# Kernel tuning notes

Hardware: AMD Instinct MI355X
Metric: run time of the kernel (lower is better)

The kernel has to match this reference:

```python
import jax, jax.numpy as jnp
import numpy as np

# Per-level grid spatial shapes: ceil([T,H,W]/grid_size/2**i) + 1 with
# video (T,H,W) = (120,1080,1920), grid_size=8, n_levels=2.
GRID_SHAPES = [jnp.array([16.0, 136.0, 241.0], dtype=jnp.float32),
               jnp.array([9.0, 69.0, 121.0], dtype=jnp.float32)]
EMB_DIM = 16
N_PTS = 1_000_000

# 8 binary corner offsets, MSB-first bit order (matches f'{i:03b}').
OFFSETS = jnp.array([[(i >> 2) & 1, (i >> 1) & 1, i & 1] for i in range(8)],
                    dtype=jnp.float32)  # [8,3]


def setup_inputs() -> dict:
    key = jax.random.key(0)
    k0, k1, k2 = jax.random.split(key, 3)
    inputs = jax.random.uniform(k0, (N_PTS, 3), dtype=jnp.float32)
    emb0 = jax.random.normal(k1, (16, 136, 241, EMB_DIM), dtype=jnp.float32)
    emb1 = jax.random.normal(k2, (9, 69, 121, EMB_DIM), dtype=jnp.float32)
    return {"inputs": inputs, "emb0": emb0, "emb1": emb1}


def _encode_level(inputs, emb, gshape):
    # inputs: [N,3] in [0,1]; emb: [T,H,W,D]; gshape: [3] float grid shape
    coords = inputs * (gshape - 1.0)                         # [N,3]
    corner = jnp.floor(coords[:, None, :] + OFFSETS)         # [N,8,3]
    corner = jnp.clip(corner, 0.0, gshape - 1.0)             # [N,8,3]
    idx = corner.astype(jnp.int32)
    values = emb[idx[..., 0], idx[..., 1], idx[..., 2]]      # [N,8,D] gather
    weights = jnp.prod(1.0 - jnp.abs(corner - coords[:, None, :]),
                       axis=-1, keepdims=True)               # [N,8,1]
    return jnp.sum(weights * values, axis=-2)                # [N,D]


def reference(inputs, emb0, emb1):
    out0 = _encode_level(inputs, emb0, GRID_SHAPES[0])
    out1 = _encode_level(inputs, emb1, GRID_SHAPES[1])
    return jnp.concatenate([out0, out1], axis=-1)            # [N, 2*D]
```

## Files before the change

### kernel.cpp

```cpp
#include <hip/hip_runtime.h>


typedef float floatx4 __attribute__((ext_vector_type(4)));

#define KXB 8
#define KYB 17
#define KZB 31
#define NBINS (KXB * KYB * KZB)
#define NSUB 4
#define CAPS 104
#define CAP_TOT (NSUB * CAPS)
#define CNT_DWORDS (NSUB * NBINS + 1)

#define L0X 3
#define L0Y 9
#define L0Z 9
#define L0CELLS (L0X * L0Y * L0Z)
#define CSTR 20

__device__ __forceinline__ int point_key(float px, float py, float pz) {
    int ix = (int)(px * 15.0f);  ix = min(max(ix, 0), 15);
    int iy = (int)(py * 135.0f); iy = min(max(iy, 0), 135);
    int iz = (int)(pz * 240.0f); iz = min(max(iz, 0), 240);
    return ((ix >> 1) * KYB + (iy >> 3)) * KZB + (iz >> 3);
}

__device__ __forceinline__ void load4pts(const float* __restrict__ pts, int i4,
                                         float px[4], float py[4], float pz[4]) {
    const floatx4* v = (const floatx4*)(pts + (size_t)i4 * 3);
    const floatx4 a = v[0], b = v[1], c = v[2];
    px[0] = a.x; py[0] = a.y; pz[0] = a.z;
    px[1] = a.w; py[1] = b.x; pz[1] = b.y;
    px[2] = b.z; py[2] = b.w; pz[2] = c.x;
    px[3] = c.y; py[3] = c.z; pz[3] = c.w;
}

__global__ __launch_bounds__(256)
void k_zero(unsigned* __restrict__ cnt) {
    const int i = blockIdx.x * blockDim.x + threadIdx.x;
    if (i < CNT_DWORDS) cnt[i] = 0u;
}

__global__ __launch_bounds__(256)
void k_bin(const float* __restrict__ pts, int n,
           unsigned* __restrict__ cnt, unsigned* __restrict__ ovfc,
           unsigned* __restrict__ slots, unsigned* __restrict__ ovf) {
    const int i4 = (blockIdx.x * blockDim.x + threadIdx.x) * 4;
    if (i4 >= n) return;
    if (i4 + 3 < n) {
        float px[4], py[4], pz[4];
        load4pts(pts, i4, px, py, pz);
        int k[4];
#pragma unroll
        for (int j = 0; j < 4; ++j) k[j] = point_key(px[j], py[j], pz[j]);
        unsigned pos[4];
#pragma unroll
        for (int j = 0; j < 4; ++j)
            pos[j] = atomicAdd(&cnt[j * NBINS + k[j]], 1u);
#pragma unroll
        for (int j = 0; j < 4; ++j) {
            if (pos[j] < CAPS)
                slots[(size_t)k[j] * CAP_TOT + j * CAPS + pos[j]] = (unsigned)(i4 + j);
            else
                ovf[atomicAdd(ovfc, 1u)] = (unsigned)(i4 + j);
        }
    } else {
        for (int j = 0; j < 4 && i4 + j < n; ++j) {
            const size_t b = (size_t)(i4 + j) * 3;
            const int k = point_key(pts[b], pts[b+1], pts[b+2]);
            const unsigned pos = atomicAdd(&cnt[j * NBINS + k], 1u);
            if (pos < CAPS) slots[(size_t)k * CAP_TOT + j * CAPS + pos] = (unsigned)(i4 + j);
            else            ovf[atomicAdd(ovfc, 1u)] = (unsigned)(i4 + j);
        }
    }
}

__device__ __forceinline__ void setup_lds(float cx, float cy, float cz,
                                          int xb, int yb, int zb, int d,
                                          int* __restrict__ off,
                                          float* __restrict__ w) {
    float gx[2] = { floorf(cx), floorf(cx + 1.0f) };
    float gy[2] = { floorf(cy), floorf(cy + 1.0f) };
    float gz[2] = { floorf(cz), floorf(cz + 1.0f) };
    float wx[2], wy[2], wz[2];
    int   xo[2], yo[2], zo[2];
#pragma unroll
    for (int b = 0; b < 2; ++b) {
        gx[b] = fminf(fmaxf(gx[b], 0.0f), 15.0f);
        gy[b] = fminf(fmaxf(gy[b], 0.0f), 135.0f);
        gz[b] = fminf(fmaxf(gz[b], 0.0f), 240.0f);
        wx[b] = 1.0f - fabsf(gx[b] - cx);
        wy[b] = 1.0f - fabsf(gy[b] - cy);
        wz[b] = 1.0f - fabsf(gz[b] - cz);
        xo[b] = min((int)gx[b] - xb, L0X - 1) * (L0Y * L0Z * CSTR);
        yo[b] = min((int)gy[b] - yb, L0Y - 1) * (L0Z * CSTR);
        zo[b] = min((int)gz[b] - zb, L0Z - 1) * CSTR + d;
    }
    float wyz[4];
    int   yzo[4];
#pragma unroll
    for (int j = 0; j < 2; ++j)
#pragma unroll
        for (int k = 0; k < 2; ++k) {
            wyz[2 * j + k] = wy[j] * wz[k];
            yzo[2 * j + k] = yo[j] + zo[k];
        }
#pragma unroll
    for (int c = 0; c < 8; ++c) {
        const int i = (c >> 2) & 1, jk = c & 3;
        w[c]   = wx[i] * wyz[jk];
        off[c] = xo[i] + yzo[jk];
    }
}

__device__ __forceinline__ void setup_glb(float cx, float cy, float cz,
                                          float tm1, float hm1, float wm1,
                                          int sh, int sw, int d,
                                          int* __restrict__ off,
                                          float* __restrict__ w) {
    float gx[2] = { floorf(cx), floorf(cx + 1.0f) };
    float gy[2] = { floorf(cy), floorf(cy + 1.0f) };
    float gz[2] = { floorf(cz), floorf(cz + 1.0f) };
    float wx[2], wy[2], wz[2];
    int   xo[2], yo[2], zo[2];
#pragma unroll
    for (int b = 0; b < 2; ++b) {
        gx[b] = fminf(fmaxf(gx[b], 0.0f), tm1);
        gy[b] = fminf(fmaxf(gy[b], 0.0f), hm1);
        gz[b] = fminf(fmaxf(gz[b], 0.0f), wm1);
        wx[b] = 1.0f - fabsf(gx[b] - cx);
        wy[b] = 1.0f - fabsf(gy[b] - cy);
        wz[b] = 1.0f - fabsf(gz[b] - cz);
        xo[b] = (int)gx[b] * sh;
        yo[b] = (int)gy[b] * sw;
        zo[b] = (int)gz[b] * 16 + d;
    }
    float wyz[4];
    int   yzo[4];
#pragma unroll
    for (int j = 0; j < 2; ++j)
#pragma unroll
        for (int k = 0; k < 2; ++k) {
            wyz[2 * j + k] = wy[j] * wz[k];
            yzo[2 * j + k] = yo[j] + zo[k];
        }
#pragma unroll
    for (int c = 0; c < 8; ++c) {
        const int i = (c >> 2) & 1, jk = c & 3;
        w[c]   = wx[i] * wyz[jk];
        off[c] = xo[i] + yzo[jk];
    }
}

__device__ __forceinline__ void encode_glb_quad(int p, int lane4,
                                                const float* __restrict__ pts,
                                                const float* __restrict__ emb0,
                                                const float* __restrict__ emb1,
                                                float* __restrict__ out) {
    const size_t b = (size_t)p * 3;
    const float px = pts[b], py = pts[b + 1], pz = pts[b + 2];
    int   o0[8], o1[8];
    float w0[8], w1[8];
    setup_glb(px * 15.0f, py * 135.0f, pz * 240.0f, 15.0f, 135.0f, 240.0f,
              136 * 241 * 16, 241 * 16, lane4, o0, w0);
    setup_glb(px * 8.0f, py * 68.0f, pz * 120.0f, 8.0f, 68.0f, 120.0f,
              69 * 121 * 16, 121 * 16, lane4, o1, w1);
    floatx4 a0 = {0,0,0,0}, a1 = {0,0,0,0};
#pragma unroll
    for (int c = 0; c < 8; ++c) a0 += w0[c] * *(const floatx4*)(emb0 + o0[c]);
#pragma unroll
    for (int c = 0; c < 8; ++c) a1 += w1[c] * *(const floatx4*)(emb1 + o1[c]);
    float* row = out + (size_t)p * 32 + lane4;
    __builtin_nontemporal_store(a0, (floatx4*)row);
    __builtin_nontemporal_store(a1, (floatx4*)(row + 16));
}

__global__ __launch_bounds__(256, 4)
void k_main_bins(const unsigned* __restrict__ slots,
                 const unsigned* __restrict__ cnt,
                 const unsigned* __restrict__ ovfc,
                 const unsigned* __restrict__ ovf,
                 const float* __restrict__ pts,
                 const float* __restrict__ emb0,
                 const float* __restrict__ emb1,
                 float* __restrict__ out) {
    const int bin = (blockIdx.x & 7) * 527 + (blockIdx.x >> 3);
    const unsigned n0 = min(cnt[bin],             (unsigned)CAPS);
    const unsigned n1 = min(cnt[NBINS + bin],     (unsigned)CAPS);
    const unsigned n2 = min(cnt[2 * NBINS + bin], (unsigned)CAPS);
    const unsigned n3 = min(cnt[3 * NBINS + bin], (unsigned)CAPS);
    const unsigned c0 = n0, c1 = c0 + n1, c2 = c1 + n2, nt = c2 + n3;

    __shared__ float lds0[L0CELLS * CSTR];

    const int tid = threadIdx.x;
    const int d = (tid & 3) * 4;

    if (nt != 0) {
        const int bz = bin % KZB;
        const int t1 = bin / KZB;
        const int by = t1 % KYB;
        const int bx = t1 / KYB;

        const int x0 = bx * 2, y0 = by * 8, z0 = bz * 8;

        for (int idx = tid; idx < L0CELLS * 4; idx += 256) {
            const int cell = idx >> 2, q = (idx & 3) * 4;
            const int lz = cell % L0Z;
            const int t = cell / L0Z;
            const int ly = t % L0Y, lx = t / L0Y;
            const int gx = min(x0 + lx, 15), gy = min(y0 + ly, 135), gz = min(z0 + lz, 240);
            const floatx4 v = *(const floatx4*)(emb0 + ((size_t)(gx * 136 + gy) * 241 + gz) * 16 + q);
            *(floatx4*)(lds0 + cell * CSTR + q) = v;
        }
        __syncthreads();

        const int quad = tid >> 2;
        const size_t sbase = (size_t)bin * CAP_TOT;

        auto slot_of = [&](unsigned t) -> unsigned {
            const unsigned seg = (t >= c0) + (t >= c1) + (t >= c2);
            const unsigned base = (seg == 0) ? 0u : ((seg == 1) ? c0 : ((seg == 2) ? c1 : c2));
            return (unsigned)(sbase + seg * CAPS + (t - base));
        };

        unsigned tA = quad, tB = quad + 64;
        int origA = (int)slots[slot_of(min(tA, nt - 1))];
        int origB = (int)slots[slot_of(min(tB, nt - 1))];
        size_t pbA = (size_t)origA * 3;
        float pxA = pts[pbA], pyA = pts[pbA + 1], pzA = pts[pbA + 2];

        while (tA < nt) {
            const unsigned tC = tB + 64;
            const int origC = (int)slots[slot_of(min(tC, nt - 1))];
            const size_t pbB = (size_t)origB * 3;
            const float pxB = pts[pbB], pyB = pts[pbB + 1], pzB = pts[pbB + 2];

            int   o0[8], o1[8];
            float w0[8], w1[8];
            setup_lds(pxA * 15.0f, pyA * 135.0f, pzA * 240.0f, x0, y0, z0, d, o0, w0);
            setup_glb(pxA * 8.0f, pyA * 68.0f, pzA * 120.0f, 8.0f, 68.0f, 120.0f,
                      69 * 121 * 16, 121 * 16, d, o1, w1);

            floatx4 v1[8];
#pragma unroll
            for (int c = 0; c < 8; ++c) v1[c] = *(const floatx4*)(emb1 + o1[c]);
            __builtin_amdgcn_sched_barrier(0);

            floatx4 a0 = {0.f, 0.f, 0.f, 0.f}, a1 = {0.f, 0.f, 0.f, 0.f};
#pragma unroll
            for (int c = 0; c < 8; ++c) a0 += w0[c] * *(const floatx4*)(lds0 + o0[c]);
#pragma unroll
            for (int c = 0; c < 8; ++c) a1 += w1[c] * v1[c];

            float* row = out + (size_t)origA * 32 + d;
            __builtin_nontemporal_store(a0, (floatx4*)row);
            __builtin_nontemporal_store(a1, (floatx4*)(row + 16));

            tA = tB; tB = tC;
            origA = origB; origB = origC;
            pxA = pxB; pyA = pyB; pzA = pzB;
        }
    }

    if (blockIdx.x < 64) {
        const unsigned total = *ovfc;
        for (unsigned i = (blockIdx.x * 256 + tid) >> 2; i < total;
             i += (64u * 256u) >> 2) {
            encode_glb_quad((int)ovf[i], d, pts, emb0, emb1, out);
        }
    }
}

__global__ __launch_bounds__(256)
void k_main_plain(const float* __restrict__ pts,
                  const float* __restrict__ emb0,
                  const float* __restrict__ emb1,
                  float* __restrict__ out, int n) {
    const int g = blockIdx.x * blockDim.x + threadIdx.x;
    const int p = g >> 2;
    if (p >= n) return;
    encode_glb_quad(p, (g & 3) * 4, pts, emb0, emb1, out);
}

extern "C" void kernel_launch(void* const* d_in, const int* in_sizes, int n_in,
                              void* d_out, int out_size, void* d_ws, size_t ws_size,
                              hipStream_t stream) {
    const float* pts  = (const float*)d_in[0];
    const float* emb0 = (const float*)d_in[1];
    const float* emb1 = (const float*)d_in[2];
    float* out = (float*)d_out;
    const int n = in_sizes[0] / 3;

    const int block = 256;
    const int n4      = (n + 3) / 4;
    const int grid_p4 = (n4 + block - 1) / block;
    const int grid_4l = (int)(((long long)n * 4 + block - 1) / block);
    const int grid_z  = (CNT_DWORDS + block - 1) / block;

    const size_t off_cnt   = 0;
    const size_t off_ovfc  = (size_t)NSUB * NBINS * 4;
    const size_t off_slots = ((off_ovfc + 4 + 31) & ~(size_t)31);
    const size_t off_ovf   = off_slots + (size_t)NBINS * CAP_TOT * 4;
    const size_t need      = off_ovf + (size_t)n * 4;

    if (ws_size < need) {
        k_main_plain<<<grid_4l, block, 0, stream>>>(pts, emb0, emb1, out, n);
        return;
    }

    char* ws = (char*)d_ws;
    unsigned* cnt   = (unsigned*)(ws + off_cnt);
    unsigned* ovfc  = (unsigned*)(ws + off_ovfc);
    unsigned* slots = (unsigned*)(ws + off_slots);
    unsigned* ovf   = (unsigned*)(ws + off_ovf);

    k_zero<<<grid_z, block, 0, stream>>>(cnt);
    k_bin<<<grid_p4, block, 0, stream>>>(pts, n, cnt, ovfc, slots, ovf);
    k_main_bins<<<NBINS, block, 0, stream>>>(slots, cnt, ovfc, ovf,
                                             pts, emb0, emb1, out);
}
```

Baseline: 111.3 us.

## Process pairs of x-adjacent bins per block with shared LDS tile and deeper prefetch

Each block now handles two bins adjacent in x, staging a larger level-0 embedding tile (5 x-planes instead of 3) in LDS once for both, which halves the block count and cuts redundant tile loads. The inner loop is restructured into a ping-pong of two point states, so the global emb1 gathers for the next point are issued before the current point is consumed. The cost is more registers per thread (two full states with 8 floatx4 each), which may reduce occupancy, plus a larger LDS footprint and fewer blocks for load balancing.

```diff
diff --git a/kernel.cpp b/kernel.cpp
--- a/kernel.cpp
+++ b/kernel.cpp
@@ -7,12 +7,13 @@
 #define KYB 17
 #define KZB 31
 #define NBINS (KXB * KYB * KZB)
+#define NPAIRS (NBINS / 2)
 #define NSUB 4
 #define CAPS 104
 #define CAP_TOT (NSUB * CAPS)
 #define CNT_DWORDS (NSUB * NBINS + 1)
 
-#define L0X 3
+#define L0X 5
 #define L0Y 9
 #define L0Z 9
 #define L0CELLS (L0X * L0Y * L0Z)
@@ -175,6 +176,43 @@
     __builtin_nontemporal_store(a1, (floatx4*)(row + 16));
 }
 
+struct PtS {
+    float   px, py, pz;
+    int     orig;
+    float   w1[8];
+    floatx4 v1[8];
+};
+
+__device__ __forceinline__ void pt_load(PtS& s, unsigned slotaddr,
+                                        const unsigned* __restrict__ slots,
+                                        const float* __restrict__ pts,
+                                        const float* __restrict__ emb1, int d) {
+    s.orig = (int)slots[slotaddr];
+    const size_t pb = (size_t)s.orig * 3;
+    s.px = pts[pb]; s.py = pts[pb + 1]; s.pz = pts[pb + 2];
+    int o1[8];
+    setup_glb(s.px * 8.0f, s.py * 68.0f, s.pz * 120.0f, 8.0f, 68.0f, 120.0f,
+              69 * 121 * 16, 121 * 16, d, o1, s.w1);
+#pragma unroll
+    for (int c = 0; c < 8; ++c) s.v1[c] = *(const floatx4*)(emb1 + o1[c]);
+}
+
+__device__ __forceinline__ void pt_consume(const PtS& s, int x0, int y0, int z0,
+                                           int d, const float* __restrict__ lds0,
+                                           float* __restrict__ out) {
+    int   o0[8];
+    float w0[8];
+    setup_lds(s.px * 15.0f, s.py * 135.0f, s.pz * 240.0f, x0, y0, z0, d, o0, w0);
+    floatx4 a0 = {0.f, 0.f, 0.f, 0.f}, a1 = {0.f, 0.f, 0.f, 0.f};
+#pragma unroll
+    for (int c = 0; c < 8; ++c) a0 += w0[c] * *(const floatx4*)(lds0 + o0[c]);
+#pragma unroll
+    for (int c = 0; c < 8; ++c) a1 += s.w1[c] * s.v1[c];
+    float* row = out + (size_t)s.orig * 32 + d;
+    __builtin_nontemporal_store(a0, (floatx4*)row);
+    __builtin_nontemporal_store(a1, (floatx4*)(row + 16));
+}
+
 __global__ __launch_bounds__(256, 4)
 void k_main_bins(const unsigned* __restrict__ slots,
                  const unsigned* __restrict__ cnt,
@@ -184,82 +222,64 @@
                  const float* __restrict__ emb0,
                  const float* __restrict__ emb1,
                  float* __restrict__ out) {
-    const int bin = (blockIdx.x & 7) * 527 + (blockIdx.x >> 3);
-    const unsigned n0 = min(cnt[bin],             (unsigned)CAPS);
-    const unsigned n1 = min(cnt[NBINS + bin],     (unsigned)CAPS);
-    const unsigned n2 = min(cnt[2 * NBINS + bin], (unsigned)CAPS);
-    const unsigned n3 = min(cnt[3 * NBINS + bin], (unsigned)CAPS);
-    const unsigned c0 = n0, c1 = c0 + n1, c2 = c1 + n2, nt = c2 + n3;
+    const int xcd = blockIdx.x & 7, ib = blockIdx.x >> 3;
+    const int pair = (xcd < 4) ? (xcd * 264 + ib) : (4 * 264 + (xcd - 4) * 263 + ib);
+
+    const int bxp  = pair / (KYB * KZB);
+    const int rest = pair % (KYB * KZB);
+    const int by = rest / KZB, bz = rest % KZB;
+    const int binA = (2 * bxp) * (KYB * KZB) + rest;
+
+    const int x0 = bxp * 4, y0 = by * 8, z0 = bz * 8;
 
     __shared__ float lds0[L0CELLS * CSTR];
 
     const int tid = threadIdx.x;
     const int d = (tid & 3) * 4;
 
-    if (nt != 0) {
-        const int bz = bin % KZB;
-        const int t1 = bin / KZB;
-        const int by = t1 % KYB;
-        const int bx = t1 / KYB;
-
-        const int x0 = bx * 2, y0 = by * 8, z0 = bz * 8;
-
-        for (int idx = tid; idx < L0CELLS * 4; idx += 256) {
-            const int cell = idx >> 2, q = (idx & 3) * 4;
-            const int lz = cell % L0Z;
-            const int t = cell / L0Z;
-            const int ly = t % L0Y, lx = t / L0Y;
-            const int gx = min(x0 + lx, 15), gy = min(y0 + ly, 135), gz = min(z0 + lz, 240);
-            const floatx4 v = *(const floatx4*)(emb0 + ((size_t)(gx * 136 + gy) * 241 + gz) * 16 + q);
-            *(floatx4*)(lds0 + cell * CSTR + q) = v;
-        }
-        __syncthreads();
-
-        const int quad = tid >> 2;
+    for (int idx = tid; idx < L0CELLS * 4; idx += 256) {
+        const int cell = idx >> 2, q = (idx & 3) * 4;
+        const int lz = cell % L0Z;
+        const int t = cell / L0Z;
+        const int ly = t % L0Y, lx = t / L0Y;
+        const int gx = min(x0 + lx, 15), gy = min(y0 + ly, 135), gz = min(z0 + lz, 240);
+        const floatx4 v = *(const floatx4*)(emb0 + ((size_t)(gx * 136 + gy) * 241 + gz) * 16 + q);
+        *(floatx4*)(lds0 + cell * CSTR + q) = v;
+    }
+    __syncthreads();
+
+    const int quad = tid >> 2;
+
+#pragma unroll 1
+    for (int sub = 0; sub < 2; ++sub) {
+        const int bin = binA + sub * (KYB * KZB);
+        const unsigned n0 = min(cnt[bin],             (unsigned)CAPS);
+        const unsigned n1 = min(cnt[NBINS + bin],     (unsigned)CAPS);
+        const unsigned n2 = min(cnt[2 * NBINS + bin], (unsigned)CAPS);
+        const unsigned n3 = min(cnt[3 * NBINS + bin], (unsigned)CAPS);
+        const unsigned c0 = n0, c1 = c0 + n1, c2 = c1 + n2, nt = c2 + n3;
+        if (nt == 0) continue;
+
         const size_t sbase = (size_t)bin * CAP_TOT;
-
         auto slot_of = [&](unsigned t) -> unsigned {
             const unsigned seg = (t >= c0) + (t >= c1) + (t >= c2);
             const unsigned base = (seg == 0) ? 0u : ((seg == 1) ? c0 : ((seg == 2) ? c1 : c2));
             return (unsigned)(sbase + seg * CAPS + (t - base));
         };
 
-        unsigned tA = quad, tB = quad + 64;
-        int origA = (int)slots[slot_of(min(tA, nt - 1))];
-        int origB = (int)slots[slot_of(min(tB, nt - 1))];
-        size_t pbA = (size_t)origA * 3;
-        float pxA = pts[pbA], pyA = pts[pbA + 1], pzA = pts[pbA + 2];
-
-        while (tA < nt) {
-            const unsigned tC = tB + 64;
-            const int origC = (int)slots[slot_of(min(tC, nt - 1))];
-            const size_t pbB = (size_t)origB * 3;
-            const float pxB = pts[pbB], pyB = pts[pbB + 1], pzB = pts[pbB + 2];
-
-            int   o0[8], o1[8];
-            float w0[8], w1[8];
-            setup_lds(pxA * 15.0f, pyA * 135.0f, pzA * 240.0f, x0, y0, z0, d, o0, w0);
-            setup_glb(pxA * 8.0f, pyA * 68.0f, pzA * 120.0f, 8.0f, 68.0f, 120.0f,
-                      69 * 121 * 16, 121 * 16, d, o1, w1);
-
-            floatx4 v1[8];
-#pragma unroll
-            for (int c = 0; c < 8; ++c) v1[c] = *(const floatx4*)(emb1 + o1[c]);
+        PtS sA, sB;
+        unsigned t = quad;
+        pt_load(sA, slot_of(min(t, nt - 1)), slots, pts, emb1, d);
+        while (t < nt) {
+            pt_load(sB, slot_of(min(t + 64, nt - 1)), slots, pts, emb1, d);
             __builtin_amdgcn_sched_barrier(0);
-
-            floatx4 a0 = {0.f, 0.f, 0.f, 0.f}, a1 = {0.f, 0.f, 0.f, 0.f};
-#pragma unroll
-            for (int c = 0; c < 8; ++c) a0 += w0[c] * *(const floatx4*)(lds0 + o0[c]);
-#pragma unroll
-            for (int c = 0; c < 8; ++c) a1 += w1[c] * v1[c];
-
-            float* row = out + (size_t)origA * 32 + d;
-            __builtin_nontemporal_store(a0, (floatx4*)row);
-            __builtin_nontemporal_store(a1, (floatx4*)(row + 16));
-
-            tA = tB; tB = tC;
-            origA = origB; origB = origC;
-            pxA = pxB; pyA = pyB; pzA = pzB;
+            pt_consume(sA, x0, y0, z0, d, lds0, out);
+            t += 64;
+            if (t >= nt) break;
+            pt_load(sA, slot_of(min(t + 64, nt - 1)), slots, pts, emb1, d);
+            __builtin_amdgcn_sched_barrier(0);
+            pt_consume(sB, x0, y0, z0, d, lds0, out);
+            t += 64;
         }
     }
 
@@ -317,6 +337,6 @@
 
     k_zero<<<grid_z, block, 0, stream>>>(cnt);
     k_bin<<<grid_p4, block, 0, stream>>>(pts, n, cnt, ovfc, slots, ovf);
-    k_main_bins<<<NBINS, block, 0, stream>>>(slots, cnt, ovfc, ovf,
-                                             pts, emb0, emb1, out);
-}
+    k_main_bins<<<NPAIRS, block, 0, stream>>>(slots, cnt, ovfc, ovf,
+                                              pts, emb0, emb1, out);
+}
```

After: 130.4 us. 1.17x slower.

## Software-pipeline level-1 gathers one iteration ahead with double-buffered registers

Applied to the files above, without the earlier changes.

Restructures the per-bin point loop into a deeper software pipeline. The level-1 emb1 gather for the next point is issued before the current point's LDS interpolation and store, using two alternating register buffers, with slot and coordinate prefetch extended to three points ahead. The aim is to hide global gather latency behind the LDS work. In exchange it uses more VGPRs, which can lower occupancy, and it computes setup_glb twice per point.

```diff
diff --git a/kernel.cpp b/kernel.cpp
--- a/kernel.cpp
+++ b/kernel.cpp
@@ -201,7 +201,6 @@
         const int t1 = bin / KZB;
         const int by = t1 % KYB;
         const int bx = t1 / KYB;
-
         const int x0 = bx * 2, y0 = by * 8, z0 = bz * 8;
 
         for (int idx = tid; idx < L0CELLS * 4; idx += 256) {
@@ -224,42 +223,68 @@
             return (unsigned)(sbase + seg * CAPS + (t - base));
         };
 
-        unsigned tA = quad, tB = quad + 64;
-        int origA = (int)slots[slot_of(min(tA, nt - 1))];
-        int origB = (int)slots[slot_of(min(tB, nt - 1))];
-        size_t pbA = (size_t)origA * 3;
-        float pxA = pts[pbA], pyA = pts[pbA + 1], pzA = pts[pbA + 2];
-
-        while (tA < nt) {
-            const unsigned tC = tB + 64;
-            const int origC = (int)slots[slot_of(min(tC, nt - 1))];
-            const size_t pbB = (size_t)origB * 3;
-            const float pxB = pts[pbB], pyB = pts[pbB + 1], pzB = pts[pbB + 2];
-
-            int   o0[8], o1[8];
+        auto consume = [&](int orig, float px_, float py_, float pz_,
+                           const floatx4* v1) {
+            int   o0[8], o1u[8];
             float w0[8], w1[8];
-            setup_lds(pxA * 15.0f, pyA * 135.0f, pzA * 240.0f, x0, y0, z0, d, o0, w0);
-            setup_glb(pxA * 8.0f, pyA * 68.0f, pzA * 120.0f, 8.0f, 68.0f, 120.0f,
-                      69 * 121 * 16, 121 * 16, d, o1, w1);
-
-            floatx4 v1[8];
-#pragma unroll
-            for (int c = 0; c < 8; ++c) v1[c] = *(const floatx4*)(emb1 + o1[c]);
-            __builtin_amdgcn_sched_barrier(0);
-
+            setup_lds(px_ * 15.0f, py_ * 135.0f, pz_ * 240.0f, x0, y0, z0, d, o0, w0);
+            setup_glb(px_ * 8.0f, py_ * 68.0f, pz_ * 120.0f, 8.0f, 68.0f, 120.0f,
+                      69 * 121 * 16, 121 * 16, d, o1u, w1);
             floatx4 a0 = {0.f, 0.f, 0.f, 0.f}, a1 = {0.f, 0.f, 0.f, 0.f};
 #pragma unroll
             for (int c = 0; c < 8; ++c) a0 += w0[c] * *(const floatx4*)(lds0 + o0[c]);
 #pragma unroll
             for (int c = 0; c < 8; ++c) a1 += w1[c] * v1[c];
-
-            float* row = out + (size_t)origA * 32 + d;
+            float* row = out + (size_t)orig * 32 + d;
             __builtin_nontemporal_store(a0, (floatx4*)row);
             __builtin_nontemporal_store(a1, (floatx4*)(row + 16));
-
-            tA = tB; tB = tC;
-            origA = origB; origB = origC;
-            pxA = pxB; pyA = pyB; pzA = pzB;
+        };
+
+        auto issue_v1 = [&](float px_, float py_, float pz_, floatx4* v1) {
+            int o1[8]; float wt[8];
+            setup_glb(px_ * 8.0f, py_ * 68.0f, pz_ * 120.0f, 8.0f, 68.0f, 120.0f,
+                      69 * 121 * 16, 121 * 16, d, o1, wt);
+#pragma unroll
+            for (int c = 0; c < 8; ++c) v1[c] = *(const floatx4*)(emb1 + o1[c]);
+        };
+
+        unsigned t = quad;
+        int origA = (int)slots[slot_of(min(t,       nt - 1))];
+        int origB = (int)slots[slot_of(min(t + 64,  nt - 1))];
+        int origC = (int)slots[slot_of(min(t + 128, nt - 1))];
+        size_t pb = (size_t)origA * 3;
+        float pxA = pts[pb], pyA = pts[pb + 1], pzA = pts[pb + 2];
+        pb = (size_t)origB * 3;
+        float pxB = pts[pb], pyB = pts[pb + 1], pzB = pts[pb + 2];
+        floatx4 v1A[8], v1B[8];
+        if (t < nt) issue_v1(pxA, pyA, pzA, v1A);
+
+        while (t < nt) {
+            {
+                const int origD = (int)slots[slot_of(min(t + 192, nt - 1))];
+                pb = (size_t)origC * 3;
+                const float pxC = pts[pb], pyC = pts[pb + 1], pzC = pts[pb + 2];
+                issue_v1(pxB, pyB, pzB, v1B);
+                __builtin_amdgcn_sched_barrier(0);
+                consume(origA, pxA, pyA, pzA, v1A);
+                origA = origB; origB = origC; origC = origD;
+                pxA = pxB; pyA = pyB; pzA = pzB;
+                pxB = pxC; pyB = pyC; pzB = pzC;
+            }
+            t += 64;
+            if (t >= nt) break;
+            {
+                const int origD = (int)slots[slot_of(min(t + 192, nt - 1))];
+                pb = (size_t)origC * 3;
+                const float pxC = pts[pb], pyC = pts[pb + 1], pzC = pts[pb + 2];
+                issue_v1(pxB, pyB, pzB, v1A);
+                __builtin_amdgcn_sched_barrier(0);
+                consume(origA, pxA, pyA, pzA, v1B);
+                origA = origB; origB = origC; origC = origD;
+                pxA = pxB; pyA = pyB; pzA = pzB;
+                pxB = pxC; pyB = pyC; pzB = pzC;
+            }
+            t += 64;
         }
     }
 
```

Measured after the change: 110.2 us. Within noise of the previous version (-1.0%).

## Pipeline level-0 LDS tile loads across four x-bins per block with producer warp

Applied to the files above, without the earlier changes.

Each block now handles four consecutive x-bins for one (y,z) column using 512 threads. A dedicated producer wavefront double-buffers the next bin's level-0 embedding tile into LDS while 448 threads encode the current bin's points. The older point prefetch and sched_barrier are dropped, and the grid shrinks from 4216 to 1054 blocks. This aims to hide the LDS staging latency and reuse block setup, at the cost of fewer blocks, a lost wavefront of compute and a barrier per bin.

```diff
diff --git a/kernel.cpp b/kernel.cpp
--- a/kernel.cpp
+++ b/kernel.cpp
@@ -7,6 +7,7 @@
 #define KYB 17
 #define KZB 31
 #define NBINS (KXB * KYB * KZB)
+#define NCOMBO (KYB * KZB)
 #define NSUB 4
 #define CAPS 104
 #define CAP_TOT (NSUB * CAPS)
@@ -17,6 +18,7 @@
 #define L0Z 9
 #define L0CELLS (L0X * L0Y * L0Z)
 #define CSTR 20
+#define NQ 112
 
 __device__ __forceinline__ int point_key(float px, float py, float pz) {
     int ix = (int)(px * 15.0f);  ix = min(max(ix, 0), 15);
@@ -175,7 +177,7 @@
     __builtin_nontemporal_store(a1, (floatx4*)(row + 16));
 }
 
-__global__ __launch_bounds__(256, 4)
+__global__ __launch_bounds__(512, 8)
 void k_main_bins(const unsigned* __restrict__ slots,
                  const unsigned* __restrict__ cnt,
                  const unsigned* __restrict__ ovfc,
@@ -184,89 +186,109 @@
                  const float* __restrict__ emb0,
                  const float* __restrict__ emb1,
                  float* __restrict__ out) {
-    const int bin = (blockIdx.x & 7) * 527 + (blockIdx.x >> 3);
-    const unsigned n0 = min(cnt[bin],             (unsigned)CAPS);
-    const unsigned n1 = min(cnt[NBINS + bin],     (unsigned)CAPS);
-    const unsigned n2 = min(cnt[2 * NBINS + bin], (unsigned)CAPS);
-    const unsigned n3 = min(cnt[3 * NBINS + bin], (unsigned)CAPS);
-    const unsigned c0 = n0, c1 = c0 + n1, c2 = c1 + n2, nt = c2 + n3;
-
-    __shared__ float lds0[L0CELLS * CSTR];
+    const int j = blockIdx.x;
+    const int combo = j >> 1, half = j & 1;
+    const int by = combo / KZB, bz = combo % KZB;
+    const int y0 = by * 8, z0 = bz * 8;
+
+    __shared__ float lds[2][L0CELLS * CSTR];
 
     const int tid = threadIdx.x;
     const int d = (tid & 3) * 4;
 
-    if (nt != 0) {
-        const int bz = bin % KZB;
-        const int t1 = bin / KZB;
-        const int by = t1 % KYB;
-        const int bx = t1 / KYB;
-
-        const int x0 = bx * 2, y0 = by * 8, z0 = bz * 8;
-
-        for (int idx = tid; idx < L0CELLS * 4; idx += 256) {
-            const int cell = idx >> 2, q = (idx & 3) * 4;
-            const int lz = cell % L0Z;
-            const int t = cell / L0Z;
-            const int ly = t % L0Y, lx = t / L0Y;
-            const int gx = min(x0 + lx, 15), gy = min(y0 + ly, 135), gz = min(z0 + lz, 240);
-            const floatx4 v = *(const floatx4*)(emb0 + ((size_t)(gx * 136 + gy) * 241 + gz) * 16 + q);
-            *(floatx4*)(lds0 + cell * CSTR + q) = v;
+    auto cell_addr = [&](int idx, int x0, int& cell, int& q) -> const floatx4* {
+        cell = idx >> 2; q = (idx & 3) * 4;
+        const int lz = cell % L0Z;
+        const int t = cell / L0Z;
+        const int ly = t % L0Y, lx = t / L0Y;
+        const int gx = min(x0 + lx, 15), gy = min(y0 + ly, 135), gz = min(z0 + lz, 240);
+        return (const floatx4*)(emb0 + ((size_t)(gx * 136 + gy) * 241 + gz) * 16 + q);
+    };
+
+    {
+        const int x0 = (half * 4) * 2;
+        for (int idx = tid; idx < L0CELLS * 4; idx += 512) {
+            int cell, q;
+            const floatx4 v = *cell_addr(idx, x0, cell, q);
+            *(floatx4*)(&lds[0][cell * CSTR + q]) = v;
+        }
+    }
+    __syncthreads();
+
+    int cur = 0;
+#pragma unroll 1
+    for (int i = 0; i < 4; ++i) {
+        const int bx = half * 4 + i;
+        const int bin = bx * NCOMBO + combo;
+
+        if (tid >= 448) {
+            if (i + 1 < 4) {
+                const int lane = tid - 448;
+                const int x0n = (bx + 1) * 2;
+                float* dst = &lds[cur ^ 1][0];
+#pragma unroll 1
+                for (int k4 = 0; k4 < 4; ++k4) {
+                    floatx4 r[4];
+                    int cells[4], qs[4];
+                    bool ok[4];
+#pragma unroll
+                    for (int s = 0; s < 4; ++s) {
+                        const int idx = lane + 64 * (k4 * 4 + s);
+                        ok[s] = idx < L0CELLS * 4;
+                        const floatx4* a = cell_addr(ok[s] ? idx : 0, x0n, cells[s], qs[s]);
+                        r[s] = *a;
+                    }
+#pragma unroll
+                    for (int s = 0; s < 4; ++s)
+                        if (ok[s]) *(floatx4*)(&dst[cells[s] * CSTR + qs[s]]) = r[s];
+                }
+            }
+        } else {
+            const unsigned n0 = min(cnt[bin],             (unsigned)CAPS);
+            const unsigned n1 = min(cnt[NBINS + bin],     (unsigned)CAPS);
+            const unsigned n2 = min(cnt[2 * NBINS + bin], (unsigned)CAPS);
+            const unsigned n3 = min(cnt[3 * NBINS + bin], (unsigned)CAPS);
+            const unsigned c0 = n0, c1 = c0 + n1, c2 = c1 + n2, nt = c2 + n3;
+            const size_t sbase = (size_t)bin * CAP_TOT;
+            const int x0 = bx * 2;
+            const float* lbuf = &lds[cur][0];
+            const int quad = tid >> 2;
+
+            for (unsigned t = quad; t < nt; t += NQ) {
+                const unsigned seg = (t >= c0) + (t >= c1) + (t >= c2);
+                const unsigned base = (seg == 0) ? 0u : ((seg == 1) ? c0 : ((seg == 2) ? c1 : c2));
+                const int orig = (int)slots[sbase + seg * CAPS + (t - base)];
+                const size_t pb = (size_t)orig * 3;
+                const float px = pts[pb], py = pts[pb + 1], pz = pts[pb + 2];
+
+                int   o0[8], o1[8];
+                float w0[8], w1[8];
+                setup_glb(px * 8.0f, py * 68.0f, pz * 120.0f, 8.0f, 68.0f, 120.0f,
+                          69 * 121 * 16, 121 * 16, d, o1, w1);
+                floatx4 v1[8];
+#pragma unroll
+                for (int c = 0; c < 8; ++c) v1[c] = *(const floatx4*)(emb1 + o1[c]);
+                setup_lds(px * 15.0f, py * 135.0f, pz * 240.0f, x0, y0, z0, d, o0, w0);
+
+                floatx4 a0 = {0.f, 0.f, 0.f, 0.f}, a1 = {0.f, 0.f, 0.f, 0.f};
+#pragma unroll
+                for (int c = 0; c < 8; ++c) a0 += w0[c] * *(const floatx4*)(lbuf + o0[c]);
+#pragma unroll
+                for (int c = 0; c < 8; ++c) a1 += w1[c] * v1[c];
+
+                float* row = out + (size_t)orig * 32 + d;
+                __builtin_nontemporal_store(a0, (floatx4*)row);
+                __builtin_nontemporal_store(a1, (floatx4*)(row + 16));
+            }
         }
         __syncthreads();
-
-        const int quad = tid >> 2;
-        const size_t sbase = (size_t)bin * CAP_TOT;
-
-        auto slot_of = [&](unsigned t) -> unsigned {
-            const unsigned seg = (t >= c0) + (t >= c1) + (t >= c2);
-            const unsigned base = (seg == 0) ? 0u : ((seg == 1) ? c0 : ((seg == 2) ? c1 : c2));
-            return (unsigned)(sbase + seg * CAPS + (t - base));
-        };
-
-        unsigned tA = quad, tB = quad + 64;
-        int origA = (int)slots[slot_of(min(tA, nt - 1))];
-        int origB = (int)slots[slot_of(min(tB, nt - 1))];
-        size_t pbA = (size_t)origA * 3;
-        float pxA = pts[pbA], pyA = pts[pbA + 1], pzA = pts[pbA + 2];
-
-        while (tA < nt) {
-            const unsigned tC = tB + 64;
-            const int origC = (int)slots[slot_of(min(tC, nt - 1))];
-            const size_t pbB = (size_t)origB * 3;
-            const float pxB = pts[pbB], pyB = pts[pbB + 1], pzB = pts[pbB + 2];
-
-            int   o0[8], o1[8];
-            float w0[8], w1[8];
-            setup_lds(pxA * 15.0f, pyA * 135.0f, pzA * 240.0f, x0, y0, z0, d, o0, w0);
-            setup_glb(pxA * 8.0f, pyA * 68.0f, pzA * 120.0f, 8.0f, 68.0f, 120.0f,
-                      69 * 121 * 16, 121 * 16, d, o1, w1);
-
-            floatx4 v1[8];
-#pragma unroll
-            for (int c = 0; c < 8; ++c) v1[c] = *(const floatx4*)(emb1 + o1[c]);
-            __builtin_amdgcn_sched_barrier(0);
-
-            floatx4 a0 = {0.f, 0.f, 0.f, 0.f}, a1 = {0.f, 0.f, 0.f, 0.f};
-#pragma unroll
-            for (int c = 0; c < 8; ++c) a0 += w0[c] * *(const floatx4*)(lds0 + o0[c]);
-#pragma unroll
-            for (int c = 0; c < 8; ++c) a1 += w1[c] * v1[c];
-
-            float* row = out + (size_t)origA * 32 + d;
-            __builtin_nontemporal_store(a0, (floatx4*)row);
-            __builtin_nontemporal_store(a1, (floatx4*)(row + 16));
-
-            tA = tB; tB = tC;
-            origA = origB; origB = origC;
-            pxA = pxB; pyA = pyB; pzA = pzB;
-        }
+        cur ^= 1;
     }
 
     if (blockIdx.x < 64) {
         const unsigned total = *ovfc;
-        for (unsigned i = (blockIdx.x * 256 + tid) >> 2; i < total;
-             i += (64u * 256u) >> 2) {
+        for (unsigned i = (blockIdx.x * 512 + tid) >> 2; i < total;
+             i += (64u * 512u) >> 2) {
             encode_glb_quad((int)ovf[i], d, pts, emb0, emb1, out);
         }
     }
@@ -317,6 +339,6 @@
 
     k_zero<<<grid_z, block, 0, stream>>>(cnt);
     k_bin<<<grid_p4, block, 0, stream>>>(pts, n, cnt, ovfc, slots, ovf);
-    k_main_bins<<<NBINS, block, 0, stream>>>(slots, cnt, ovfc, ovf,
-                                             pts, emb0, emb1, out);
-}
+    k_main_bins<<<2 * NCOMBO, 512, 0, stream>>>(slots, cnt, ovfc, ovf,
+                                                pts, emb0, emb1, out);
+}
```

Result: slower. 115.4 us (+3.7%).
